# Kernel optimization log

Measured on AMD Instinct MI355X. Metric: run time of the kernel, lower is better.

## Reference

```python
import jax, jax.numpy as jnp
import numpy as np

B = 2048
V = 50257
T = 64
D = 32
N_IN = 128
N_OUT = 128
N_HID = 1500
N_LAYERS = 5
N_BIAS = 2
K = 45  # int(edge_prob * n_nodes) fixed in-degree per receiving node
HID_PER_LAYER = N_HID // N_LAYERS  # 300
N_RECV = N_HID + N_OUT  # 1628 receiving nodes (hidden + output)


def _build_graph(rng):
    """Topological random wiring: each receiving node picks K predecessors
    among all earlier nodes (inputs, bias, earlier hidden layers)."""
    src_rows = []
    avail = N_IN + N_BIAS  # nodes available before first hidden layer
    for _ in range(N_LAYERS):
        src_rows.append(rng.integers(0, avail, size=(HID_PER_LAYER, K)))
        avail += HID_PER_LAYER
    src_rows.append(rng.integers(0, avail, size=(N_OUT, K)))  # output nodes
    return np.concatenate(src_rows, axis=0).astype(np.int32)  # [N_RECV, K]


def setup_inputs() -> dict:
    key = jax.random.key(0)
    ks = jax.random.split(key, 6)
    rng = np.random.default_rng(0)
    ids = jax.random.randint(ks[0], (B, T), 0, V, dtype=jnp.int32)
    token_emb = jax.random.normal(ks[1], (V, D), dtype=jnp.float32) * 0.02
    in_w = jax.random.normal(ks[2], (N_IN, T * D), dtype=jnp.float32) / np.sqrt(T * D)
    in_b = jnp.zeros((N_IN,), dtype=jnp.float32)
    src_idx = jnp.asarray(_build_graph(rng))  # [N_RECV, K] int32
    rwnn_w = jax.random.normal(ks[3], (N_RECV, K), dtype=jnp.float32) / np.sqrt(K)
    out_w = jax.random.normal(ks[4], (V, N_OUT), dtype=jnp.float32) / np.sqrt(N_OUT)
    out_b = jnp.zeros((V,), dtype=jnp.float32)
    return {"ids": ids, "token_emb": token_emb, "in_w": in_w, "in_b": in_b,
            "src_idx": src_idx, "rwnn_w": rwnn_w, "out_w": out_w, "out_b": out_b}


def _rwnn_forward(x, src_idx, rwnn_w):
    """x: [B, N_IN] -> [B, N_OUT]. Sparse random-wired DAG forward."""
    b = x.shape[0]
    vals = jnp.concatenate([x, jnp.ones((b, N_BIAS), dtype=x.dtype)], axis=1)
    off = 0
    for _ in range(N_LAYERS):
        s = src_idx[off:off + HID_PER_LAYER]          # [300, K]
        w = rwnn_w[off:off + HID_PER_LAYER]           # [300, K]
        gathered = vals[:, s]                          # [B, 300, K] irregular gather
        new = jnp.tanh(jnp.einsum('bnk,nk->bn', gathered, w))
        vals = jnp.concatenate([vals, new], axis=1)
        off += HID_PER_LAYER
    s = src_idx[off:off + N_OUT]
    w = rwnn_w[off:off + N_OUT]
    return jnp.tanh(jnp.einsum('bnk,nk->bn', vals[:, s], w))  # [B, N_OUT]


def reference(ids, token_emb, in_w, in_b, src_idx, rwnn_w, out_w, out_b):
    emb = token_emb[ids]                     # [B, T, D]
    flat = emb.reshape(emb.shape[0], T * D)  # [B, T*D]
    x = flat @ in_w.T + in_b                 # [B, N_IN]
    h = _rwnn_forward(x, src_idx, rwnn_w)    # [B, N_OUT]
    logits = h @ out_w.T + out_b             # [B, V]
    return logits
```

## Files before the change

### kernel.cpp

```cpp
#include <hip/hip_runtime.h>

#define B_SZ   2048
#define V_SZ   50257
#define TD     2048
#define NIN    128
#define NOUT   128
#define NRECV  1628
#define KDEG   45
#define KPAD   48
#define HPL    300
#define VALSN  1632

typedef __bf16 bf16x8 __attribute__((ext_vector_type(8)));
typedef float  floatx16 __attribute__((ext_vector_type(16)));

__device__ __forceinline__ unsigned short f2bf(float f) {
  unsigned u = __float_as_uint(f);
  u += 0x7fffu + ((u >> 16) & 1u);
  return (unsigned short)(u >> 16);
}

__device__ __forceinline__ float tanh_fast(float v) {
  float e = __builtin_amdgcn_exp2f(v * 2.88539008177793f);
  return 1.0f - 2.0f * __builtin_amdgcn_rcpf(1.0f + e);
}

#define P0 1048576
#define P1 1608224
#define P2 65536
#define P4 78144
#define PREP_TOTAL (P0 + P1 + P2 + P4)
#define PREP_BLOCKS ((PREP_TOTAL + 255) / 256)

__global__ __launch_bounds__(256) void prep_kernel(
    const int* __restrict__ ids, const float* __restrict__ temb,
    const float* __restrict__ in_w,
    const int* __restrict__ src, const float* __restrict__ rw,
    const float* __restrict__ out_w,
    unsigned short* __restrict__ flatb, unsigned short* __restrict__ inwb,
    unsigned short* __restrict__ outwb,
    int* __restrict__ iw) {
  int i = blockIdx.x * 256 + threadIdx.x;
  if (i < P0) {
    int bt = i >> 3, d4 = i & 7;
    int id = ids[bt];
    float4 v = *(const float4*)(temb + id * 32 + d4 * 4);
    ushort4 o; o.x = f2bf(v.x); o.y = f2bf(v.y); o.z = f2bf(v.z); o.w = f2bf(v.w);
    *(ushort4*)(flatb + (size_t)i * 4) = o;
    return;
  }
  i -= P0;
  if (i < P1) {
    float4 v = ((const float4*)out_w)[i];
    ushort4 o; o.x = f2bf(v.x); o.y = f2bf(v.y); o.z = f2bf(v.z); o.w = f2bf(v.w);
    *(ushort4*)(outwb + (size_t)i * 4) = o;
    return;
  }
  i -= P1;
  if (i < P2) {
    float4 v = ((const float4*)in_w)[i];
    ushort4 o; o.x = f2bf(v.x); o.y = f2bf(v.y); o.z = f2bf(v.z); o.w = f2bf(v.w);
    *(ushort4*)(inwb + (size_t)i * 4) = o;
    return;
  }
  i -= P2;
  if (i < P4) {
    int r = i / KPAD, k = i - r * KPAD;
    int idx = 0; unsigned wb = 0;
    if (k < KDEG) {
      idx = src[r * KDEG + k];
      wb = __float_as_uint(rw[r * KDEG + k]);
    }
    iw[(size_t)i * 2] = idx;
    iw[(size_t)i * 2 + 1] = (int)wb;
  }
}

__global__ __launch_bounds__(256) void gemm1_kernel(
    const __bf16* __restrict__ flatb, const __bf16* __restrict__ inwb,
    const float* __restrict__ in_b, float* __restrict__ x) {
  __shared__ float red[4 * 32 * 32];
  int tid = threadIdx.x;
  int wv = tid >> 6, lane = tid & 63;
  int row = lane & 31, half = lane >> 5;
  int m0 = blockIdx.x * 32;
  int n0 = blockIdx.y * 32;
  int k0 = wv * 512;
  const __bf16* ap = flatb + (size_t)(m0 + row) * TD + k0 + half * 8;
  const __bf16* bp = inwb + (size_t)(n0 + row) * TD + k0 + half * 8;
  floatx16 acc = (floatx16)0.0f;
#pragma unroll 8
  for (int s = 0; s < 32; ++s) {
    bf16x8 a = *(const bf16x8*)(ap + s * 16);
    bf16x8 b = *(const bf16x8*)(bp + s * 16);
    acc = __builtin_amdgcn_mfma_f32_32x32x16_bf16(a, b, acc, 0, 0, 0);
  }
#pragma unroll
  for (int r = 0; r < 16; ++r) {
    int mrow = (r & 3) + 8 * (r >> 2) + 4 * half;
    red[wv * 1024 + mrow * 32 + row] = acc[r];
  }
  __syncthreads();
#pragma unroll
  for (int p = 0; p < 4; ++p) {
    int idx = p * 256 + tid;
    int ml = idx >> 5, nl = idx & 31;
    float s = red[idx] + red[1024 + idx] + red[2048 + idx] + red[3072 + idx]
            + in_b[n0 + nl];
    x[(size_t)(m0 + ml) * NIN + n0 + nl] = s;
  }
}

__global__ __launch_bounds__(512) void rwnn_kernel(
    const float* __restrict__ x, const int* __restrict__ iw,
    unsigned short* __restrict__ hb) {
  __shared__ float vals[VALSN * 8];
  int tid = threadIdx.x;
  int b0 = blockIdx.x * 8;
  {
    int p = tid & 7, n = tid >> 3;
    vals[n * 8 + p] = x[(b0 + p) * NIN + n];
    vals[(n + 64) * 8 + p] = x[(b0 + p) * NIN + n + 64];
    if (tid < 16) vals[(NIN + (tid >> 3)) * 8 + (tid & 7)] = 1.0f;
  }
  __syncthreads();
  int g = tid >> 2;
  int pq = (tid & 3) * 2;
  int base = NIN + 2;
  int off = 0;
  for (int layer = 0; layer < 5; ++layer) {
    for (int r = g; r < HPL; r += 128) {
      const int4* q4 = (const int4*)(iw) + (size_t)(off + r) * (KPAD / 2);
      float s0 = 0.f, s1 = 0.f;
#pragma unroll
      for (int k4 = 0; k4 < KPAD / 2; ++k4) {
        int4 q = q4[k4];
        float2 v0 = *(const float2*)(&vals[q.x * 8 + pq]);
        float w0 = __int_as_float(q.y);
        s0 += v0.x * w0; s1 += v0.y * w0;
        float2 v1 = *(const float2*)(&vals[q.z * 8 + pq]);
        float w1 = __int_as_float(q.w);
        s0 += v1.x * w1; s1 += v1.y * w1;
      }
      float2 o; o.x = tanh_fast(s0); o.y = tanh_fast(s1);
      *(float2*)(&vals[(base + r) * 8 + pq]) = o;
    }
    __syncthreads();
    off += HPL; base += HPL;
  }
  {
    int r = g;
    const int4* q4 = (const int4*)(iw) + (size_t)(off + r) * (KPAD / 2);
    float s0 = 0.f, s1 = 0.f;
#pragma unroll
    for (int k4 = 0; k4 < KPAD / 2; ++k4) {
      int4 q = q4[k4];
      float2 v0 = *(const float2*)(&vals[q.x * 8 + pq]);
      float w0 = __int_as_float(q.y);
      s0 += v0.x * w0; s1 += v0.y * w0;
      float2 v1 = *(const float2*)(&vals[q.z * 8 + pq]);
      float w1 = __int_as_float(q.w);
      s0 += v1.x * w1; s1 += v1.y * w1;
    }
    hb[(b0 + pq + 0) * NOUT + r] = f2bf(tanh_fast(s0));
    hb[(b0 + pq + 1) * NOUT + r] = f2bf(tanh_fast(s1));
  }
}

__global__ __launch_bounds__(256) void gemm3_kernel(
    const __bf16* __restrict__ h, const __bf16* __restrict__ wv,
    const float* __restrict__ out_b, float* __restrict__ out) {
  int tid = threadIdx.x;
  int wvid = tid >> 6, lane = tid & 63;
  int row = lane & 31, half = lane >> 5;
  int m0 = blockIdx.x * 32;
  int v0 = blockIdx.y * 128 + wvid * 32;
  int vr = v0 + row;
  int vc = vr < V_SZ ? vr : V_SZ - 1;
  const __bf16* ap = h + (size_t)(m0 + row) * NOUT + half * 8;
  const __bf16* bp = wv + (size_t)vc * NOUT + half * 8;
  floatx16 acc = (floatx16)0.0f;
#pragma unroll
  for (int s = 0; s < 8; ++s) {
    bf16x8 a = *(const bf16x8*)(ap + s * 16);
    bf16x8 b = *(const bf16x8*)(bp + s * 16);
    acc = __builtin_amdgcn_mfma_f32_32x32x16_bf16(a, b, acc, 0, 0, 0);
  }
  if (vr < V_SZ) {
    float bias = out_b[vr];
#pragma unroll
    for (int r = 0; r < 16; ++r) {
      int mrow = (r & 3) + 8 * (r >> 2) + 4 * half;
      out[(size_t)(m0 + mrow) * V_SZ + vr] = acc[r] + bias;
    }
  }
}

extern "C" void kernel_launch(void* const* d_in, const int* in_sizes, int n_in,
                              void* d_out, int out_size, void* d_ws, size_t ws_size,
                              hipStream_t stream) {
  const int*   ids   = (const int*)d_in[0];
  const float* temb  = (const float*)d_in[1];
  const float* in_w  = (const float*)d_in[2];
  const float* in_b  = (const float*)d_in[3];
  const int*   src   = (const int*)d_in[4];
  const float* rw    = (const float*)d_in[5];
  const float* out_w = (const float*)d_in[6];
  const float* out_b = (const float*)d_in[7];
  float* out = (float*)d_out;

  char* ws = (char*)d_ws;
  unsigned short* flatb = (unsigned short*)(ws);
  unsigned short* inwb  = (unsigned short*)(ws + 8388608);
  unsigned short* outwb = (unsigned short*)(ws + 8912896);
  float*          x     = (float*)(ws + 21778688);
  unsigned short* hb    = (unsigned short*)(ws + 22827264);
  int*            iw    = (int*)(ws + 23351552);

  prep_kernel<<<PREP_BLOCKS, 256, 0, stream>>>(ids, temb, in_w, src, rw,
                                               out_w, flatb, inwb, outwb, iw);
  gemm1_kernel<<<dim3(64, 4), 256, 0, stream>>>((const __bf16*)flatb,
                                                (const __bf16*)inwb, in_b, x);
  rwnn_kernel<<<256, 512, 0, stream>>>(x, iw, hb);
  gemm3_kernel<<<dim3(64, 393), 256, 0, stream>>>((const __bf16*)hb,
                                                  (const __bf16*)outwb, out_b, out);
}
```

Before: 633.5 us.

## Fuse embedding gather into input GEMM and reuse weight fragments in output GEMM

The embedding gather and bf16 conversion move out of the prep kernel into the first GEMM, which now reads token embeddings straight from the table, so the intermediate flattened buffer is never written or re-read. Each GEMM1 wave now owns a 32-column slice and runs the full K range, so the shared-memory split-K reduction and its barrier go away, but the grid shrinks to 64 blocks. The output GEMM keeps its weight fragments in registers across four 32-row M tiles and writes logits with nontemporal stores, cutting weight reloads and cache pollution. The trade-off is less parallelism in GEMM1 and more register pressure in GEMM3.

After: 752.1 us. 1.19x slower.

```diff
diff --git a/kernel.cpp b/kernel.cpp
--- a/kernel.cpp
+++ b/kernel.cpp
@@ -25,31 +25,26 @@
   return 1.0f - 2.0f * __builtin_amdgcn_rcpf(1.0f + e);
 }
 
-#define P0 1048576
+__device__ __forceinline__ bf16x8 cvt8(float4 lo, float4 hi) {
+  bf16x8 d;
+  d[0] = (__bf16)lo.x; d[1] = (__bf16)lo.y; d[2] = (__bf16)lo.z; d[3] = (__bf16)lo.w;
+  d[4] = (__bf16)hi.x; d[5] = (__bf16)hi.y; d[6] = (__bf16)hi.z; d[7] = (__bf16)hi.w;
+  return d;
+}
+
 #define P1 1608224
 #define P2 65536
 #define P4 78144
-#define PREP_TOTAL (P0 + P1 + P2 + P4)
+#define PREP_TOTAL (P1 + P2 + P4)
 #define PREP_BLOCKS ((PREP_TOTAL + 255) / 256)
 
 __global__ __launch_bounds__(256) void prep_kernel(
-    const int* __restrict__ ids, const float* __restrict__ temb,
     const float* __restrict__ in_w,
     const int* __restrict__ src, const float* __restrict__ rw,
     const float* __restrict__ out_w,
-    unsigned short* __restrict__ flatb, unsigned short* __restrict__ inwb,
-    unsigned short* __restrict__ outwb,
+    unsigned short* __restrict__ inwb, unsigned short* __restrict__ outwb,
     int* __restrict__ iw) {
   int i = blockIdx.x * 256 + threadIdx.x;
-  if (i < P0) {
-    int bt = i >> 3, d4 = i & 7;
-    int id = ids[bt];
-    float4 v = *(const float4*)(temb + id * 32 + d4 * 4);
-    ushort4 o; o.x = f2bf(v.x); o.y = f2bf(v.y); o.z = f2bf(v.z); o.w = f2bf(v.w);
-    *(ushort4*)(flatb + (size_t)i * 4) = o;
-    return;
-  }
-  i -= P0;
   if (i < P1) {
     float4 v = ((const float4*)out_w)[i];
     ushort4 o; o.x = f2bf(v.x); o.y = f2bf(v.y); o.z = f2bf(v.z); o.w = f2bf(v.w);
@@ -77,37 +72,42 @@
 }
 
 __global__ __launch_bounds__(256) void gemm1_kernel(
-    const __bf16* __restrict__ flatb, const __bf16* __restrict__ inwb,
-    const float* __restrict__ in_b, float* __restrict__ x) {
-  __shared__ float red[4 * 32 * 32];
+    const int* __restrict__ ids, const float* __restrict__ temb,
+    const __bf16* __restrict__ inwb, const float* __restrict__ in_b,
+    float* __restrict__ x) {
   int tid = threadIdx.x;
   int wv = tid >> 6, lane = tid & 63;
   int row = lane & 31, half = lane >> 5;
   int m0 = blockIdx.x * 32;
-  int n0 = blockIdx.y * 32;
-  int k0 = wv * 512;
-  const __bf16* ap = flatb + (size_t)(m0 + row) * TD + k0 + half * 8;
-  const __bf16* bp = inwb + (size_t)(n0 + row) * TD + k0 + half * 8;
+  int n0 = wv * 32;
+  const int4* idq = (const int4*)(ids + (size_t)(m0 + row) * 64);
+  const __bf16* bp = inwb + (size_t)(n0 + row) * TD + half * 8;
   floatx16 acc = (floatx16)0.0f;
-#pragma unroll 8
-  for (int s = 0; s < 32; ++s) {
-    bf16x8 a = *(const bf16x8*)(ap + s * 16);
-    bf16x8 b = *(const bf16x8*)(bp + s * 16);
-    acc = __builtin_amdgcn_mfma_f32_32x32x16_bf16(a, b, acc, 0, 0, 0);
-  }
+  for (int t4 = 0; t4 < 16; ++t4) {
+    int4 iq = idq[t4];
+#pragma unroll
+    for (int j = 0; j < 4; ++j) {
+      int id = (j == 0) ? iq.x : (j == 1) ? iq.y : (j == 2) ? iq.z : iq.w;
+      int t = t4 * 4 + j;
+      const float* tp = temb + (size_t)id * 32;
+      float4 a0 = *(const float4*)(tp + 8 * half);
+      float4 a1 = *(const float4*)(tp + 8 * half + 4);
+      float4 a2 = *(const float4*)(tp + 16 + 8 * half);
+      float4 a3 = *(const float4*)(tp + 16 + 8 * half + 4);
+      bf16x8 av0 = cvt8(a0, a1);
+      bf16x8 av1 = cvt8(a2, a3);
+      bf16x8 b0 = *(const bf16x8*)(bp + t * 32);
+      bf16x8 b1 = *(const bf16x8*)(bp + t * 32 + 16);
+      acc = __builtin_amdgcn_mfma_f32_32x32x16_bf16(av0, b0, acc, 0, 0, 0);
+      acc = __builtin_amdgcn_mfma_f32_32x32x16_bf16(av1, b1, acc, 0, 0, 0);
+    }
+  }
+  int col = n0 + row;
+  float bias = in_b[col];
 #pragma unroll
   for (int r = 0; r < 16; ++r) {
     int mrow = (r & 3) + 8 * (r >> 2) + 4 * half;
-    red[wv * 1024 + mrow * 32 + row] = acc[r];
-  }
-  __syncthreads();
-#pragma unroll
-  for (int p = 0; p < 4; ++p) {
-    int idx = p * 256 + tid;
-    int ml = idx >> 5, nl = idx & 31;
-    float s = red[idx] + red[1024 + idx] + red[2048 + idx] + red[3072 + idx]
-            + in_b[n0 + nl];
-    x[(size_t)(m0 + ml) * NIN + n0 + nl] = s;
+    x[(size_t)(m0 + mrow) * NIN + col] = acc[r] + bias;
   }
 }
 
@@ -173,25 +173,31 @@
   int tid = threadIdx.x;
   int wvid = tid >> 6, lane = tid & 63;
   int row = lane & 31, half = lane >> 5;
-  int m0 = blockIdx.x * 32;
+  int m0 = blockIdx.x * 128;
   int v0 = blockIdx.y * 128 + wvid * 32;
   int vr = v0 + row;
   int vc = vr < V_SZ ? vr : V_SZ - 1;
-  const __bf16* ap = h + (size_t)(m0 + row) * NOUT + half * 8;
   const __bf16* bp = wv + (size_t)vc * NOUT + half * 8;
-  floatx16 acc = (floatx16)0.0f;
-#pragma unroll
-  for (int s = 0; s < 8; ++s) {
-    bf16x8 a = *(const bf16x8*)(ap + s * 16);
-    bf16x8 b = *(const bf16x8*)(bp + s * 16);
-    acc = __builtin_amdgcn_mfma_f32_32x32x16_bf16(a, b, acc, 0, 0, 0);
-  }
-  if (vr < V_SZ) {
-    float bias = out_b[vr];
-#pragma unroll
-    for (int r = 0; r < 16; ++r) {
-      int mrow = (r & 3) + 8 * (r >> 2) + 4 * half;
-      out[(size_t)(m0 + mrow) * V_SZ + vr] = acc[r] + bias;
+  bf16x8 bfrag[8];
+#pragma unroll
+  for (int s = 0; s < 8; ++s) bfrag[s] = *(const bf16x8*)(bp + s * 16);
+  float bias = (vr < V_SZ) ? out_b[vr] : 0.f;
+#pragma unroll
+  for (int mt = 0; mt < 4; ++mt) {
+    const __bf16* ap = h + (size_t)(m0 + mt * 32 + row) * NOUT + half * 8;
+    floatx16 acc = (floatx16)0.0f;
+#pragma unroll
+    for (int s = 0; s < 8; ++s) {
+      bf16x8 a = *(const bf16x8*)(ap + s * 16);
+      acc = __builtin_amdgcn_mfma_f32_32x32x16_bf16(a, bfrag[s], acc, 0, 0, 0);
+    }
+    if (vr < V_SZ) {
+#pragma unroll
+      for (int r = 0; r < 16; ++r) {
+        int mrow = (r & 3) + 8 * (r >> 2) + 4 * half;
+        __builtin_nontemporal_store(acc[r] + bias,
+            &out[(size_t)(m0 + mt * 32 + mrow) * V_SZ + vr]);
+      }
     }
   }
 }
@@ -210,18 +216,16 @@
   float* out = (float*)d_out;
 
   char* ws = (char*)d_ws;
-  unsigned short* flatb = (unsigned short*)(ws);
   unsigned short* inwb  = (unsigned short*)(ws + 8388608);
   unsigned short* outwb = (unsigned short*)(ws + 8912896);
   float*          x     = (float*)(ws + 21778688);
   unsigned short* hb    = (unsigned short*)(ws + 22827264);
   int*            iw    = (int*)(ws + 23351552);
 
-  prep_kernel<<<PREP_BLOCKS, 256, 0, stream>>>(ids, temb, in_w, src, rw,
-                                               out_w, flatb, inwb, outwb, iw);
-  gemm1_kernel<<<dim3(64, 4), 256, 0, stream>>>((const __bf16*)flatb,
-                                                (const __bf16*)inwb, in_b, x);
+  prep_kernel<<<PREP_BLOCKS, 256, 0, stream>>>(in_w, src, rw, out_w,
+                                               inwb, outwb, iw);
+  gemm1_kernel<<<64, 256, 0, stream>>>(ids, temb, (const __bf16*)inwb, in_b, x);
   rwnn_kernel<<<256, 512, 0, stream>>>(x, iw, hb);
-  gemm3_kernel<<<dim3(64, 393), 256, 0, stream>>>((const __bf16*)hb,
+  gemm3_kernel<<<dim3(16, 393), 256, 0, stream>>>((const __bf16*)hb,
                                                   (const __bf16*)outwb, out_b, out);
 }
```
